# Performance work log

Hardware: AMD Instinct MI355X
Metric: run time of the kernel (lower is better)

## Reference

```python
import jax, jax.numpy as jnp
import numpy as np

BATCH, SEQ, EMBED = 4, 4096, 512
NUM_HEADS = 8
D_K = EMBED // NUM_HEADS  # = n_wires of the quantum layer


def setup_inputs() -> dict:
    key = jax.random.key(0)
    k1, k2, k3, k4 = jax.random.split(key, 4)
    x = jax.random.normal(k1, (BATCH, SEQ, EMBED), dtype=jnp.float32)
    theta = jax.random.normal(k2, (D_K,), dtype=jnp.float32)          # trainable RX angles (shared across heads)
    W_out = jax.random.normal(k3, (EMBED, EMBED), dtype=jnp.float32) * (1.0 / np.sqrt(EMBED))
    b_out = jax.random.normal(k4, (EMBED,), dtype=jnp.float32) * 0.01
    return {"x": x, "theta": theta, "W_out": W_out, "b_out": b_out}


def reference(x, theta, W_out, b_out):
    b, s, e = x.shape
    d_k = theta.shape[0]
    h = e // d_k
    # Quantum stage: per wire, RX(x_i) then RX(theta_i) on |0>, measure PauliZ.
    # RX gates on the same wire compose, and <Z| RX(phi)|0> state> = cos(phi),
    # so the whole per-head circuit is elementwise cos(x + theta).
    xh = x.reshape(b, s, h, d_k)                 # split heads
    q_concat = jnp.cos(xh + theta).reshape(b, s, e)
    # q = k = v = out_proj(q_concat)  (same Linear applied three times)
    q = q_concat @ W_out.T + b_out               # [b, s, e]
    scale = 1.0 / jnp.sqrt(jnp.asarray(d_k, dtype=q.dtype))
    scores = jax.nn.softmax(jnp.einsum('bie,bje->bij', q, q) * scale, axis=-1)  # [b, s, s]
    out = jnp.einsum('bij,bje->bie', scores, q)  # dropout = identity (inference)
    return out
```

## Files before the change

kernel.cpp:

```cpp
#include <hip/hip_runtime.h>

typedef __bf16 bf16_t;
typedef bf16_t bf16x8 __attribute__((ext_vector_type(8)));
typedef bf16_t bf16x4 __attribute__((ext_vector_type(4)));
typedef float f32x4 __attribute__((ext_vector_type(4)));

#define BATCH 4
#define SEQ 4096
#define EMBED 512
#define MTOT (BATCH * SEQ)
#define NSPLIT 2
#define KT (SEQ / NSPLIT)
#define BC 32
#define FITERS (KT / BC)

__device__ float  Lacc_g[MTOT];
__device__ bf16_t Wbf_g[EMBED * EMBED];

__device__ __forceinline__ void async_copy16(const bf16_t* g, bf16_t* l) {
    __builtin_amdgcn_global_load_lds(
        (const __attribute__((address_space(1))) unsigned int*)g,
        (__attribute__((address_space(3))) unsigned int*)l, 16, 0, 0);
}

__global__ __launch_bounds__(256) void cvt_w_kernel(const float* __restrict__ W) {
    const int i = (blockIdx.x * 256 + threadIdx.x) * 4;
    float4 v = *(const float4*)&W[i];
    bf16x4 o;
    o[0] = (bf16_t)v.x; o[1] = (bf16_t)v.y; o[2] = (bf16_t)v.z; o[3] = (bf16_t)v.w;
    *(bf16x4*)&Wbf_g[i] = o;
}

__global__ __launch_bounds__(256, 2) void gemm_q_kernel(
    const float* __restrict__ x, const float* __restrict__ theta,
    const float* __restrict__ bias,
    bf16_t* __restrict__ kperm, bf16_t* __restrict__ qt)
{
    __shared__ alignas(16) bf16_t As[32][40];
    __shared__ alignas(16) bf16_t Ws[512][40];
    __shared__ float th[64];

    const int t    = threadIdx.x;
    const int m0   = blockIdx.x * 32;
    const int lane = t & 63;
    const int wave = t >> 6;
    const int l15  = lane & 15;
    const int quad = lane >> 4;

    if (t < 64) th[t] = theta[t];
    if (blockIdx.x < 16)
        ((float4*)Lacc_g)[blockIdx.x * 256 + t] = make_float4(0.f, 0.f, 0.f, 0.f);

    f32x4 acc[2][8];
#pragma unroll
    for (int m = 0; m < 2; ++m)
#pragma unroll
        for (int n = 0; n < 8; ++n) acc[m][n] = (f32x4){0.f, 0.f, 0.f, 0.f};

    const int arow = t >> 3;
    const int aseg = t & 7;

    for (int kk = 0; kk < 16; ++kk) {
        const int k0 = kk * 32;
        __syncthreads();
        {
            float4 xv = *(const float4*)&x[(m0 + arow) * 512 + k0 + aseg * 4];
            bf16x4 av;
            av[0] = (bf16_t)__cosf(xv.x + th[(k0 + aseg * 4 + 0) & 63]);
            av[1] = (bf16_t)__cosf(xv.y + th[(k0 + aseg * 4 + 1) & 63]);
            av[2] = (bf16_t)__cosf(xv.z + th[(k0 + aseg * 4 + 2) & 63]);
            av[3] = (bf16_t)__cosf(xv.w + th[(k0 + aseg * 4 + 3) & 63]);
            *(bf16x4*)&As[arow][aseg * 4] = av;
        }
#pragma unroll
        for (int cc = 0; cc < 8; ++cc) {
            int idx = t + 256 * cc;
            int row = idx >> 2;
            int seg = idx & 3;
            *(bf16x8*)&Ws[row][seg * 8] =
                *(const bf16x8*)&Wbf_g[row * 512 + k0 + seg * 8];
        }
        __syncthreads();
        bf16x8 af[2];
#pragma unroll
        for (int m = 0; m < 2; ++m)
            af[m] = *(const bf16x8*)&As[m * 16 + l15][quad * 8];
#pragma unroll
        for (int n = 0; n < 8; ++n) {
            bf16x8 bfr = *(const bf16x8*)&Ws[wave * 128 + n * 16 + l15][quad * 8];
#pragma unroll
            for (int m = 0; m < 2; ++m)
                acc[m][n] = __builtin_amdgcn_mfma_f32_16x16x32_bf16(af[m], bfr, acc[m][n], 0, 0, 0);
        }
    }

#pragma unroll
    for (int n = 0; n < 8; ++n) {
        const int col = wave * 128 + n * 16 + l15;
        const float bv = bias[col];
        const int kf = col >> 5;
        const int qk = (col >> 3) & 3;
        const int jj = col & 7;
#pragma unroll
        for (int m = 0; m < 2; ++m) {
            const int row0 = m0 + m * 16 + quad * 4;
            const int b    = row0 >> 12;
            const int i0   = row0 & 4095;
            const int tile = i0 >> 5;
            const size_t kb = (size_t)b * (SEQ * EMBED) + (size_t)tile * 16384
                            + (size_t)(m * 16 + kf) * 512 + qk * 128
                            + (quad * 4) * 8 + jj;
            bf16x4 pack;
#pragma unroll
            for (int r = 0; r < 4; ++r) {
                bf16_t qv = (bf16_t)(acc[m][n][r] + bv);
                kperm[kb + r * 8] = qv;
                pack[r] = qv;
            }
            *(bf16x4*)&qt[((size_t)(b * 512 + col) << 12) + i0] = pack;
        }
    }
}

__global__ __launch_bounds__(256, 2) void flash_kernel(
    const bf16_t* __restrict__ kp, const bf16_t* __restrict__ qt,
    float* __restrict__ out)
{
    __shared__ alignas(16) bf16_t Ks[2][32 * 512];
    __shared__ alignas(16) bf16_t Ps[2][4 * 512];

    const int t    = threadIdx.x;
    const int lane = t & 63;
    const int wave = t >> 6;
    const int l15  = lane & 15;
    const int quad = lane >> 4;

    const int L      = blockIdx.x;
    const int g      = L & 7;
    const int qtile  = L >> 3;
    const int batch  = g >> 1;
    const int ksplit = g & 1;

    const int q0     = qtile * 64;
    const int kbase  = ksplit * KT;
    const int ktile0 = kbase >> 5;
    const bf16_t* kpb = kp + (size_t)batch * SEQ * EMBED;
    const bf16_t* qtb = qt + (size_t)batch * EMBED * SEQ;

#pragma unroll
    for (int cc = 0; cc < 8; ++cc) {
        const int f = cc * 4 + wave;
        async_copy16(&kpb[(size_t)ktile0 * 16384 + f * 512 + lane * 8],
                     &Ks[0][f * 512]);
    }

    bf16x8 bQ[16];
    {
        const size_t qb = (size_t)(qtile * 2 + (wave >> 1)) * 16384
                        + (size_t)(wave & 1) * 16 * 512;
#pragma unroll
        for (int kf = 0; kf < 16; ++kf)
            bQ[kf] = *(const bf16x8*)&kpb[qb + kf * 512 + quad * 128 + l15 * 8];
    }

    f32x4 O[4][8];
#pragma unroll
    for (int m = 0; m < 4; ++m)
#pragma unroll
        for (int n = 0; n < 8; ++n) O[m][n] = (f32x4){0.f, 0.f, 0.f, 0.f};
    float lpart = 0.f;

    for (int it = 0; it < FITERS; ++it) {
        const int cbuf = it & 1;
        const int pbuf = cbuf ^ 1;
        __syncthreads();
        if (it + 1 < FITERS) {
#pragma unroll
            for (int cc = 0; cc < 8; ++cc) {
                const int f = cc * 4 + wave;
                async_copy16(&kpb[(size_t)(ktile0 + it + 1) * 16384 + f * 512 + lane * 8],
                             &Ks[pbuf][f * 512]);
            }
        }
        bf16x8 bv[8];
        if (it) {
            const int kv = kbase + (it - 1) * BC;
#pragma unroll
            for (int n = 0; n < 8; ++n)
                bv[n] = *(const bf16x8*)&qtb[(size_t)(wave * 128 + n * 16 + l15) * 4096
                                             + kv + quad * 8];
        }
        f32x4 s[2];
#pragma unroll
        for (int kt = 0; kt < 2; ++kt) {
            f32x4 a = (f32x4){0.f, 0.f, 0.f, 0.f};
#pragma unroll
            for (int kf = 0; kf < 16; ++kf) {
                bf16x8 ak = *(const bf16x8*)&Ks[cbuf][(kt * 16 + kf) * 512 + lane * 8];
                a = __builtin_amdgcn_mfma_f32_16x16x32_bf16(ak, bQ[kf], a, 0, 0, 0);
            }
            s[kt] = a;
        }
#pragma unroll
        for (int kt = 0; kt < 2; ++kt) {
            bf16x4 pk;
#pragma unroll
            for (int r = 0; r < 4; ++r) {
                bf16_t pb = (bf16_t)__expf(s[kt][r] * 0.125f);
                lpart += (float)pb;
                pk[r] = pb;
            }
            *(bf16x4*)&Ps[cbuf][wave * 512 + (kt * 2 + (quad >> 1)) * 128
                                + l15 * 8 + (quad & 1) * 4] = pk;
        }
        if (it) {
            bf16x8 pa[4];
#pragma unroll
            for (int mt = 0; mt < 4; ++mt)
                pa[mt] = *(const bf16x8*)&Ps[pbuf][mt * 512 + lane * 8];
#pragma unroll
            for (int n = 0; n < 8; ++n)
#pragma unroll
                for (int mt = 0; mt < 4; ++mt)
                    O[mt][n] = __builtin_amdgcn_mfma_f32_16x16x32_bf16(pa[mt], bv[n], O[mt][n], 0, 0, 0);
        }
    }
    __syncthreads();
    {
        const int pbuf = (FITERS - 1) & 1;
        const int kv = kbase + (FITERS - 1) * BC;
        bf16x8 bv[8];
#pragma unroll
        for (int n = 0; n < 8; ++n)
            bv[n] = *(const bf16x8*)&qtb[(size_t)(wave * 128 + n * 16 + l15) * 4096
                                         + kv + quad * 8];
        bf16x8 pa[4];
#pragma unroll
        for (int mt = 0; mt < 4; ++mt)
            pa[mt] = *(const bf16x8*)&Ps[pbuf][mt * 512 + lane * 8];
#pragma unroll
        for (int n = 0; n < 8; ++n)
#pragma unroll
            for (int mt = 0; mt < 4; ++mt)
                O[mt][n] = __builtin_amdgcn_mfma_f32_16x16x32_bf16(pa[mt], bv[n], O[mt][n], 0, 0, 0);
    }

    {
        float ls = lpart;
        ls += __shfl_xor(ls, 16);
        ls += __shfl_xor(ls, 32);
        if (quad == 0)
            atomicAdd(&Lacc_g[batch * SEQ + q0 + wave * 16 + l15], ls);
    }
#pragma unroll
    for (int mt = 0; mt < 4; ++mt)
#pragma unroll
        for (int r = 0; r < 4; ++r) {
            const size_t row = (size_t)batch * SEQ + q0 + mt * 16 + quad * 4 + r;
#pragma unroll
            for (int n = 0; n < 8; ++n)
                atomicAdd(&out[row * 512 + wave * 128 + n * 16 + l15], O[mt][n][r]);
        }
}

__global__ __launch_bounds__(256) void norm_kernel(float* __restrict__ out)
{
    const int idx = blockIdx.x * 256 + threadIdx.x;
    float4 v = ((float4*)out)[idx];
    const float inv = 1.0f / Lacc_g[idx >> 7];
    v.x *= inv; v.y *= inv; v.z *= inv; v.w *= inv;
    ((float4*)out)[idx] = v;
}

extern "C" void kernel_launch(void* const* d_in, const int* in_sizes, int n_in,
                              void* d_out, int out_size, void* d_ws, size_t ws_size,
                              hipStream_t stream) {
    const float* x     = (const float*)d_in[0];
    const float* theta = (const float*)d_in[1];
    const float* W     = (const float*)d_in[2];
    const float* bias  = (const float*)d_in[3];
    float* out    = (float*)d_out;
    bf16_t* kperm = (bf16_t*)d_ws;
    bf16_t* qt    = kperm + (size_t)MTOT * EMBED;

    hipMemsetAsync(out, 0, (size_t)MTOT * EMBED * sizeof(float), stream);

    cvt_w_kernel<<<dim3(EMBED * EMBED / 4 / 256), dim3(256), 0, stream>>>(W);

    gemm_q_kernel<<<dim3(MTOT / 32), dim3(256), 0, stream>>>(x, theta, bias, kperm, qt);

    flash_kernel<<<dim3(64 * BATCH * NSPLIT), dim3(256), 0, stream>>>(kperm, qt, out);

    norm_kernel<<<dim3(MTOT * EMBED / 4 / 256), dim3(256), 0, stream>>>(out);
}
```

Baseline: 392.7 us.

## Replace output atomics with per-split buffers, add MFMA priority and dual accumulators

When the workspace is large enough, each key-split block writes its partial output to its own fp32 buffer with plain stores, and the normalize kernel sums the two buffers. This removes the memset and the float atomics on the output. The flash loop also issues the V loads before the async K copy, splits the QK reduction into two independent accumulator chains, and raises wave priority around the MFMA blocks. The cost is 64 MB of extra workspace traffic, and whether the new path runs depends on ws_size.

```diff
diff --git a/kernel.cpp b/kernel.cpp
--- a/kernel.cpp
+++ b/kernel.cpp
@@ -124,7 +124,7 @@
 
 __global__ __launch_bounds__(256, 2) void flash_kernel(
     const bf16_t* __restrict__ kp, const bf16_t* __restrict__ qt,
-    float* __restrict__ out)
+    float* __restrict__ out, float* __restrict__ obuf, const int split)
 {
     __shared__ alignas(16) bf16_t Ks[2][32 * 512];
     __shared__ alignas(16) bf16_t Ps[2][4 * 512];
@@ -174,6 +174,14 @@
         const int cbuf = it & 1;
         const int pbuf = cbuf ^ 1;
         __syncthreads();
+        bf16x8 bv[8];
+        if (it) {
+            const int kv = kbase + (it - 1) * BC;
+#pragma unroll
+            for (int n = 0; n < 8; ++n)
+                bv[n] = *(const bf16x8*)&qtb[(size_t)(wave * 128 + n * 16 + l15) * 4096
+                                             + kv + quad * 8];
+        }
         if (it + 1 < FITERS) {
 #pragma unroll
             for (int cc = 0; cc < 8; ++cc) {
@@ -182,25 +190,22 @@
                              &Ks[pbuf][f * 512]);
             }
         }
-        bf16x8 bv[8];
-        if (it) {
-            const int kv = kbase + (it - 1) * BC;
-#pragma unroll
-            for (int n = 0; n < 8; ++n)
-                bv[n] = *(const bf16x8*)&qtb[(size_t)(wave * 128 + n * 16 + l15) * 4096
-                                             + kv + quad * 8];
-        }
         f32x4 s[2];
+        __builtin_amdgcn_s_setprio(1);
 #pragma unroll
         for (int kt = 0; kt < 2; ++kt) {
-            f32x4 a = (f32x4){0.f, 0.f, 0.f, 0.f};
-#pragma unroll
-            for (int kf = 0; kf < 16; ++kf) {
-                bf16x8 ak = *(const bf16x8*)&Ks[cbuf][(kt * 16 + kf) * 512 + lane * 8];
-                a = __builtin_amdgcn_mfma_f32_16x16x32_bf16(ak, bQ[kf], a, 0, 0, 0);
-            }
-            s[kt] = a;
-        }
+            f32x4 a0 = (f32x4){0.f, 0.f, 0.f, 0.f};
+            f32x4 a1 = (f32x4){0.f, 0.f, 0.f, 0.f};
+#pragma unroll
+            for (int kf = 0; kf < 8; ++kf) {
+                bf16x8 ak0 = *(const bf16x8*)&Ks[cbuf][(kt * 16 + kf) * 512 + lane * 8];
+                bf16x8 ak1 = *(const bf16x8*)&Ks[cbuf][(kt * 16 + 8 + kf) * 512 + lane * 8];
+                a0 = __builtin_amdgcn_mfma_f32_16x16x32_bf16(ak0, bQ[kf],     a0, 0, 0, 0);
+                a1 = __builtin_amdgcn_mfma_f32_16x16x32_bf16(ak1, bQ[8 + kf], a1, 0, 0, 0);
+            }
+            s[kt] = a0 + a1;
+        }
+        __builtin_amdgcn_s_setprio(0);
 #pragma unroll
         for (int kt = 0; kt < 2; ++kt) {
             bf16x4 pk;
@@ -218,11 +223,13 @@
 #pragma unroll
             for (int mt = 0; mt < 4; ++mt)
                 pa[mt] = *(const bf16x8*)&Ps[pbuf][mt * 512 + lane * 8];
+            __builtin_amdgcn_s_setprio(1);
 #pragma unroll
             for (int n = 0; n < 8; ++n)
 #pragma unroll
                 for (int mt = 0; mt < 4; ++mt)
                     O[mt][n] = __builtin_amdgcn_mfma_f32_16x16x32_bf16(pa[mt], bv[n], O[mt][n], 0, 0, 0);
+            __builtin_amdgcn_s_setprio(0);
         }
     }
     __syncthreads();
@@ -238,11 +245,13 @@
 #pragma unroll
         for (int mt = 0; mt < 4; ++mt)
             pa[mt] = *(const bf16x8*)&Ps[pbuf][mt * 512 + lane * 8];
+        __builtin_amdgcn_s_setprio(1);
 #pragma unroll
         for (int n = 0; n < 8; ++n)
 #pragma unroll
             for (int mt = 0; mt < 4; ++mt)
                 O[mt][n] = __builtin_amdgcn_mfma_f32_16x16x32_bf16(pa[mt], bv[n], O[mt][n], 0, 0, 0);
+        __builtin_amdgcn_s_setprio(0);
     }
 
     {
@@ -252,21 +261,42 @@
         if (quad == 0)
             atomicAdd(&Lacc_g[batch * SEQ + q0 + wave * 16 + l15], ls);
     }
-#pragma unroll
-    for (int mt = 0; mt < 4; ++mt)
-#pragma unroll
-        for (int r = 0; r < 4; ++r) {
-            const size_t row = (size_t)batch * SEQ + q0 + mt * 16 + quad * 4 + r;
-#pragma unroll
-            for (int n = 0; n < 8; ++n)
-                atomicAdd(&out[row * 512 + wave * 128 + n * 16 + l15], O[mt][n][r]);
-        }
-}
-
-__global__ __launch_bounds__(256) void norm_kernel(float* __restrict__ out)
+    if (split) {
+        float* ob = obuf + (size_t)ksplit * MTOT * EMBED;
+#pragma unroll
+        for (int mt = 0; mt < 4; ++mt)
+#pragma unroll
+            for (int r = 0; r < 4; ++r) {
+                const size_t row = (size_t)batch * SEQ + q0 + mt * 16 + quad * 4 + r;
+#pragma unroll
+                for (int n = 0; n < 8; ++n)
+                    ob[row * 512 + wave * 128 + n * 16 + l15] = O[mt][n][r];
+            }
+    } else {
+#pragma unroll
+        for (int mt = 0; mt < 4; ++mt)
+#pragma unroll
+            for (int r = 0; r < 4; ++r) {
+                const size_t row = (size_t)batch * SEQ + q0 + mt * 16 + quad * 4 + r;
+#pragma unroll
+                for (int n = 0; n < 8; ++n)
+                    atomicAdd(&out[row * 512 + wave * 128 + n * 16 + l15], O[mt][n][r]);
+            }
+    }
+}
+
+__global__ __launch_bounds__(256) void norm_kernel(
+    float* __restrict__ out, const float* __restrict__ obuf, const int split)
 {
     const int idx = blockIdx.x * 256 + threadIdx.x;
-    float4 v = ((float4*)out)[idx];
+    float4 v;
+    if (split) {
+        float4 a = ((const float4*)obuf)[idx];
+        float4 b = ((const float4*)(obuf + (size_t)MTOT * EMBED))[idx];
+        v = make_float4(a.x + b.x, a.y + b.y, a.z + b.z, a.w + b.w);
+    } else {
+        v = ((float4*)out)[idx];
+    }
     const float inv = 1.0f / Lacc_g[idx >> 7];
     v.x *= inv; v.y *= inv; v.z *= inv; v.w *= inv;
     ((float4*)out)[idx] = v;
@@ -282,14 +312,19 @@
     float* out    = (float*)d_out;
     bf16_t* kperm = (bf16_t*)d_ws;
     bf16_t* qt    = kperm + (size_t)MTOT * EMBED;
-
-    hipMemsetAsync(out, 0, (size_t)MTOT * EMBED * sizeof(float), stream);
+    float*  obuf  = (float*)(qt + (size_t)MTOT * EMBED);
+
+    const size_t need = (size_t)MTOT * EMBED * (2 + 2 + 8);
+    const int split = (ws_size >= need) ? 1 : 0;
+
+    if (!split)
+        hipMemsetAsync(out, 0, (size_t)MTOT * EMBED * sizeof(float), stream);
 
     cvt_w_kernel<<<dim3(EMBED * EMBED / 4 / 256), dim3(256), 0, stream>>>(W);
 
     gemm_q_kernel<<<dim3(MTOT / 32), dim3(256), 0, stream>>>(x, theta, bias, kperm, qt);
 
-    flash_kernel<<<dim3(64 * BATCH * NSPLIT), dim3(256), 0, stream>>>(kperm, qt, out);
-
-    norm_kernel<<<dim3(MTOT * EMBED / 4 / 256), dim3(256), 0, stream>>>(out);
-}
+    flash_kernel<<<dim3(64 * BATCH * NSPLIT), dim3(256), 0, stream>>>(kperm, qt, out, obuf, split);
+
+    norm_kernel<<<dim3(MTOT * EMBED / 4 / 256), dim3(256), 0, stream>>>(out, obuf, split);
+}
```

Measured after the change: 462.0 us. 17.7% more time.

## Retile projection GEMM to 128x128 with async LDS loads; tune flash inner loop

Applied to the files above, without the earlier changes.

Moves the cos(x+theta) computation into a separate elementwise kernel that writes a bf16 activation buffer. The projection GEMM is retiled from 32x512 to 128x128 blocks with 64-wide K steps, loaded through direct global-to-LDS async copies, which improves operand reuse. In the flash kernel the V loads are hoisted ahead of the K prefetch, the QK dot product is split into two independent MFMA accumulator chains, and MFMA sections run at raised wave priority. The cost is an extra kernel launch plus a bf16 activation round trip through memory, and the new GEMM LDS layout is unpadded, which may cause bank conflicts.

```diff
diff --git a/kernel.cpp b/kernel.cpp
--- a/kernel.cpp
+++ b/kernel.cpp
@@ -29,91 +29,103 @@
     bf16x4 o;
     o[0] = (bf16_t)v.x; o[1] = (bf16_t)v.y; o[2] = (bf16_t)v.z; o[3] = (bf16_t)v.w;
     *(bf16x4*)&Wbf_g[i] = o;
+    if (blockIdx.x < 16)
+        ((float4*)Lacc_g)[blockIdx.x * 256 + threadIdx.x] = make_float4(0.f, 0.f, 0.f, 0.f);
+}
+
+__global__ __launch_bounds__(256) void cvt_a_kernel(
+    const float* __restrict__ x, const float* __restrict__ theta,
+    bf16_t* __restrict__ abuf)
+{
+    const int i = (blockIdx.x * 256 + threadIdx.x) * 8;
+    float4 a = *(const float4*)&x[i];
+    float4 b = *(const float4*)&x[i + 4];
+    const int e0 = i & 63;
+    bf16x8 o;
+    o[0] = (bf16_t)__cosf(a.x + theta[e0 + 0]);
+    o[1] = (bf16_t)__cosf(a.y + theta[e0 + 1]);
+    o[2] = (bf16_t)__cosf(a.z + theta[e0 + 2]);
+    o[3] = (bf16_t)__cosf(a.w + theta[e0 + 3]);
+    o[4] = (bf16_t)__cosf(b.x + theta[e0 + 4]);
+    o[5] = (bf16_t)__cosf(b.y + theta[e0 + 5]);
+    o[6] = (bf16_t)__cosf(b.z + theta[e0 + 6]);
+    o[7] = (bf16_t)__cosf(b.w + theta[e0 + 7]);
+    *(bf16x8*)&abuf[i] = o;
 }
 
 __global__ __launch_bounds__(256, 2) void gemm_q_kernel(
-    const float* __restrict__ x, const float* __restrict__ theta,
-    const float* __restrict__ bias,
+    const bf16_t* __restrict__ abuf, const float* __restrict__ bias,
     bf16_t* __restrict__ kperm, bf16_t* __restrict__ qt)
 {
-    __shared__ alignas(16) bf16_t As[32][40];
-    __shared__ alignas(16) bf16_t Ws[512][40];
-    __shared__ float th[64];
+    __shared__ alignas(16) bf16_t As[128 * 64];
+    __shared__ alignas(16) bf16_t Bs[128 * 64];
 
     const int t    = threadIdx.x;
-    const int m0   = blockIdx.x * 32;
     const int lane = t & 63;
     const int wave = t >> 6;
     const int l15  = lane & 15;
     const int quad = lane >> 4;
-
-    if (t < 64) th[t] = theta[t];
-    if (blockIdx.x < 16)
-        ((float4*)Lacc_g)[blockIdx.x * 256 + t] = make_float4(0.f, 0.f, 0.f, 0.f);
-
-    f32x4 acc[2][8];
-#pragma unroll
-    for (int m = 0; m < 2; ++m)
-#pragma unroll
-        for (int n = 0; n < 8; ++n) acc[m][n] = (f32x4){0.f, 0.f, 0.f, 0.f};
-
-    const int arow = t >> 3;
-    const int aseg = t & 7;
-
-    for (int kk = 0; kk < 16; ++kk) {
-        const int k0 = kk * 32;
+    const int m0   = (blockIdx.x >> 2) * 128;
+    const int n0   = (blockIdx.x & 3) * 128;
+    const int wm   = wave >> 1;
+    const int wn   = wave & 1;
+
+    const int drow = lane >> 3;
+    const int dseg = lane & 7;
+
+    f32x4 acc[4][4];
+#pragma unroll
+    for (int mt = 0; mt < 4; ++mt)
+#pragma unroll
+        for (int nt = 0; nt < 4; ++nt) acc[mt][nt] = (f32x4){0.f, 0.f, 0.f, 0.f};
+
+    for (int kk = 0; kk < 8; ++kk) {
+        const int k0 = kk * 64;
         __syncthreads();
-        {
-            float4 xv = *(const float4*)&x[(m0 + arow) * 512 + k0 + aseg * 4];
-            bf16x4 av;
-            av[0] = (bf16_t)__cosf(xv.x + th[(k0 + aseg * 4 + 0) & 63]);
-            av[1] = (bf16_t)__cosf(xv.y + th[(k0 + aseg * 4 + 1) & 63]);
-            av[2] = (bf16_t)__cosf(xv.z + th[(k0 + aseg * 4 + 2) & 63]);
-            av[3] = (bf16_t)__cosf(xv.w + th[(k0 + aseg * 4 + 3) & 63]);
-            *(bf16x4*)&As[arow][aseg * 4] = av;
-        }
-#pragma unroll
-        for (int cc = 0; cc < 8; ++cc) {
-            int idx = t + 256 * cc;
-            int row = idx >> 2;
-            int seg = idx & 3;
-            *(bf16x8*)&Ws[row][seg * 8] =
-                *(const bf16x8*)&Wbf_g[row * 512 + k0 + seg * 8];
+#pragma unroll
+        for (int j = 0; j < 4; ++j) {
+            const int c   = wave * 4 + j;
+            const int row = c * 8 + drow;
+            async_copy16(&abuf[(size_t)(m0 + row) * 512 + k0 + dseg * 8], &As[c * 512]);
+            async_copy16(&Wbf_g[(size_t)(n0 + row) * 512 + k0 + dseg * 8], &Bs[c * 512]);
         }
         __syncthreads();
-        bf16x8 af[2];
-#pragma unroll
-        for (int m = 0; m < 2; ++m)
-            af[m] = *(const bf16x8*)&As[m * 16 + l15][quad * 8];
-#pragma unroll
-        for (int n = 0; n < 8; ++n) {
-            bf16x8 bfr = *(const bf16x8*)&Ws[wave * 128 + n * 16 + l15][quad * 8];
-#pragma unroll
-            for (int m = 0; m < 2; ++m)
-                acc[m][n] = __builtin_amdgcn_mfma_f32_16x16x32_bf16(af[m], bfr, acc[m][n], 0, 0, 0);
-        }
-    }
-
-#pragma unroll
-    for (int n = 0; n < 8; ++n) {
-        const int col = wave * 128 + n * 16 + l15;
+#pragma unroll
+        for (int kh = 0; kh < 2; ++kh) {
+            bf16x8 af[4], bfr[4];
+#pragma unroll
+            for (int i = 0; i < 4; ++i) {
+                af[i]  = *(const bf16x8*)&As[(wm * 64 + i * 16 + l15) * 64 + kh * 32 + quad * 8];
+                bfr[i] = *(const bf16x8*)&Bs[(wn * 64 + i * 16 + l15) * 64 + kh * 32 + quad * 8];
+            }
+#pragma unroll
+            for (int mt = 0; mt < 4; ++mt)
+#pragma unroll
+                for (int nt = 0; nt < 4; ++nt)
+                    acc[mt][nt] = __builtin_amdgcn_mfma_f32_16x16x32_bf16(af[mt], bfr[nt], acc[mt][nt], 0, 0, 0);
+        }
+    }
+
+#pragma unroll
+    for (int nt = 0; nt < 4; ++nt) {
+        const int col = n0 + wn * 64 + nt * 16 + l15;
         const float bv = bias[col];
         const int kf = col >> 5;
         const int qk = (col >> 3) & 3;
         const int jj = col & 7;
 #pragma unroll
-        for (int m = 0; m < 2; ++m) {
-            const int row0 = m0 + m * 16 + quad * 4;
+        for (int mt = 0; mt < 4; ++mt) {
+            const int row0 = m0 + wm * 64 + mt * 16 + quad * 4;
             const int b    = row0 >> 12;
             const int i0   = row0 & 4095;
             const int tile = i0 >> 5;
             const size_t kb = (size_t)b * (SEQ * EMBED) + (size_t)tile * 16384
-                            + (size_t)(m * 16 + kf) * 512 + qk * 128
-                            + (quad * 4) * 8 + jj;
+                            + (size_t)(((i0 >> 4) & 1) * 16 + kf) * 512 + qk * 128
+                            + (i0 & 15) * 8 + jj;
             bf16x4 pack;
 #pragma unroll
             for (int r = 0; r < 4; ++r) {
-                bf16_t qv = (bf16_t)(acc[m][n][r] + bv);
+                bf16_t qv = (bf16_t)(acc[mt][nt][r] + bv);
                 kperm[kb + r * 8] = qv;
                 pack[r] = qv;
             }
@@ -174,6 +186,14 @@
         const int cbuf = it & 1;
         const int pbuf = cbuf ^ 1;
         __syncthreads();
+        bf16x8 bv[8];
+        if (it) {
+            const int kv = kbase + (it - 1) * BC;
+#pragma unroll
+            for (int n = 0; n < 8; ++n)
+                bv[n] = *(const bf16x8*)&qtb[(size_t)(wave * 128 + n * 16 + l15) * 4096
+                                             + kv + quad * 8];
+        }
         if (it + 1 < FITERS) {
 #pragma unroll
             for (int cc = 0; cc < 8; ++cc) {
@@ -182,25 +202,22 @@
                              &Ks[pbuf][f * 512]);
             }
         }
-        bf16x8 bv[8];
-        if (it) {
-            const int kv = kbase + (it - 1) * BC;
-#pragma unroll
-            for (int n = 0; n < 8; ++n)
-                bv[n] = *(const bf16x8*)&qtb[(size_t)(wave * 128 + n * 16 + l15) * 4096
-                                             + kv + quad * 8];
-        }
         f32x4 s[2];
+        __builtin_amdgcn_s_setprio(1);
 #pragma unroll
         for (int kt = 0; kt < 2; ++kt) {
-            f32x4 a = (f32x4){0.f, 0.f, 0.f, 0.f};
-#pragma unroll
-            for (int kf = 0; kf < 16; ++kf) {
-                bf16x8 ak = *(const bf16x8*)&Ks[cbuf][(kt * 16 + kf) * 512 + lane * 8];
-                a = __builtin_amdgcn_mfma_f32_16x16x32_bf16(ak, bQ[kf], a, 0, 0, 0);
-            }
-            s[kt] = a;
-        }
+            f32x4 a0 = (f32x4){0.f, 0.f, 0.f, 0.f};
+            f32x4 a1 = (f32x4){0.f, 0.f, 0.f, 0.f};
+#pragma unroll
+            for (int kf = 0; kf < 8; ++kf) {
+                bf16x8 ak0 = *(const bf16x8*)&Ks[cbuf][(kt * 16 + kf) * 512 + lane * 8];
+                bf16x8 ak1 = *(const bf16x8*)&Ks[cbuf][(kt * 16 + 8 + kf) * 512 + lane * 8];
+                a0 = __builtin_amdgcn_mfma_f32_16x16x32_bf16(ak0, bQ[kf],     a0, 0, 0, 0);
+                a1 = __builtin_amdgcn_mfma_f32_16x16x32_bf16(ak1, bQ[8 + kf], a1, 0, 0, 0);
+            }
+            s[kt] = a0 + a1;
+        }
+        __builtin_amdgcn_s_setprio(0);
 #pragma unroll
         for (int kt = 0; kt < 2; ++kt) {
             bf16x4 pk;
@@ -218,11 +235,13 @@
 #pragma unroll
             for (int mt = 0; mt < 4; ++mt)
                 pa[mt] = *(const bf16x8*)&Ps[pbuf][mt * 512 + lane * 8];
+            __builtin_amdgcn_s_setprio(1);
 #pragma unroll
             for (int n = 0; n < 8; ++n)
 #pragma unroll
                 for (int mt = 0; mt < 4; ++mt)
                     O[mt][n] = __builtin_amdgcn_mfma_f32_16x16x32_bf16(pa[mt], bv[n], O[mt][n], 0, 0, 0);
+            __builtin_amdgcn_s_setprio(0);
         }
     }
     __syncthreads();
@@ -238,11 +257,13 @@
 #pragma unroll
         for (int mt = 0; mt < 4; ++mt)
             pa[mt] = *(const bf16x8*)&Ps[pbuf][mt * 512 + lane * 8];
+        __builtin_amdgcn_s_setprio(1);
 #pragma unroll
         for (int n = 0; n < 8; ++n)
 #pragma unroll
             for (int mt = 0; mt < 4; ++mt)
                 O[mt][n] = __builtin_amdgcn_mfma_f32_16x16x32_bf16(pa[mt], bv[n], O[mt][n], 0, 0, 0);
+        __builtin_amdgcn_s_setprio(0);
     }
 
     {
@@ -282,12 +303,15 @@
     float* out    = (float*)d_out;
     bf16_t* kperm = (bf16_t*)d_ws;
     bf16_t* qt    = kperm + (size_t)MTOT * EMBED;
+    bf16_t* abuf  = qt + (size_t)MTOT * EMBED;
 
     hipMemsetAsync(out, 0, (size_t)MTOT * EMBED * sizeof(float), stream);
 
     cvt_w_kernel<<<dim3(EMBED * EMBED / 4 / 256), dim3(256), 0, stream>>>(W);
 
-    gemm_q_kernel<<<dim3(MTOT / 32), dim3(256), 0, stream>>>(x, theta, bias, kperm, qt);
+    cvt_a_kernel<<<dim3(MTOT * EMBED / 8 / 256), dim3(256), 0, stream>>>(x, theta, abuf);
+
+    gemm_q_kernel<<<dim3((MTOT / 128) * 4), dim3(256), 0, stream>>>(abuf, bias, kperm, qt);
 
     flash_kernel<<<dim3(64 * BATCH * NSPLIT), dim3(256), 0, stream>>>(kperm, qt, out);
 
```

After: 479.4 us. 22.1% more time.
